# Kernel tuning notes

Hardware: AMD Instinct MI355X
Metric: run time of the kernel (lower is better)

## Reference

```python
import jax, jax.numpy as jnp
import numpy as np

N = 100000
E = 3200000
F_IN = 27
H1, C1 = 8, 8
H2, C2 = 1, 2
NEG_SLOPE = 0.2


def gat_conv(x, src, dst, W, a_src, a_dst, b, heads, ch, n_nodes):
    # x: [N, F_in]; src/dst: [E'] (self-loops already appended)
    h = (x @ W).reshape(n_nodes, heads, ch)            # [N, H, C]
    alpha_src = jnp.sum(h * a_src, axis=-1)            # [N, H]
    alpha_dst = jnp.sum(h * a_dst, axis=-1)            # [N, H]
    e = jax.nn.leaky_relu(alpha_src[src] + alpha_dst[dst], NEG_SLOPE)  # [E', H]
    m = jax.ops.segment_max(e, dst, num_segments=n_nodes)             # [N, H]
    ex = jnp.exp(e - m[dst])
    denom = jax.ops.segment_sum(ex, dst, num_segments=n_nodes)        # [N, H]
    alpha = ex / denom[dst]                                           # [E', H]
    out = jax.ops.segment_sum(h[src] * alpha[:, :, None], dst, num_segments=n_nodes)
    return out.reshape(n_nodes, heads * ch) + b


def setup_inputs() -> dict:
    key = jax.random.key(0)
    ks = jax.random.split(key, 10)
    x = jax.random.normal(ks[0], (N, F_IN), dtype=jnp.float32)
    edge_index = jax.random.randint(ks[1], (2, E), 0, N, dtype=jnp.int64)
    s1 = 1.0 / np.sqrt(F_IN)
    s2 = 1.0 / np.sqrt(H1 * C1)
    W1 = jax.random.uniform(ks[2], (F_IN, H1 * C1), jnp.float32, -s1, s1)
    a_src1 = jax.random.uniform(ks[3], (H1, C1), jnp.float32, -s1, s1)
    a_dst1 = jax.random.uniform(ks[4], (H1, C1), jnp.float32, -s1, s1)
    b1 = jnp.zeros((H1 * C1,), jnp.float32)
    W2 = jax.random.uniform(ks[5], (H1 * C1, H2 * C2), jnp.float32, -s2, s2)
    a_src2 = jax.random.uniform(ks[6], (H2, C2), jnp.float32, -s2, s2)
    a_dst2 = jax.random.uniform(ks[7], (H2, C2), jnp.float32, -s2, s2)
    b2 = jnp.zeros((H2 * C2,), jnp.float32)
    return {"x": x, "edge_index": edge_index, "W1": W1, "a_src1": a_src1,
            "a_dst1": a_dst1, "b1": b1, "W2": W2, "a_src2": a_src2,
            "a_dst2": a_dst2, "b2": b2}


def reference(x, edge_index, W1, a_src1, a_dst1, b1, W2, a_src2, a_dst2, b2):
    # eval mode: dropouts are identity. PyG GATConv adds self-loops by default.
    loop = jnp.arange(N, dtype=edge_index.dtype)
    src = jnp.concatenate([edge_index[0], loop])
    dst = jnp.concatenate([edge_index[1], loop])
    h = jax.nn.elu(gat_conv(x, src, dst, W1, a_src1, a_dst1, b1, H1, C1, N))
    out = gat_conv(h, src, dst, W2, a_src2, a_dst2, b2, H2, C2, N)
    return jax.nn.log_softmax(out, axis=1)
```

## Files before the change

### kernel.cpp

```cpp
#include <hip/hip_runtime.h>
#include <hip/hip_fp16.h>
#include <math.h>

#define NN 100000
#define EE 3200000
#define ET (EE + NN)

#define H1n 8
#define C1n 8
#define F1n 64
#define FINn 27
#define NEG 0.2f

#define NPB 128
#define NB 782
#define STRIDE 5120
#define TILE 4096
#define ABLK 256
#define WIN (STRIDE + NPB)
#define FBLK 512
#define RPT 10

typedef float floatx2 __attribute__((ext_vector_type(2)));

static __device__ __forceinline__ float lrelu(float v) {
    return v > 0.f ? v : NEG * v;
}

__global__ __launch_bounds__(ABLK) void k_binA(const int* __restrict__ ei,
                                               int* __restrict__ tail,
                                               int* __restrict__ recs) {
    __shared__ int hist[NB];
    __shared__ int lofs[NB];
    __shared__ int cur[NB];
    __shared__ int gpos[NB];
    __shared__ int sorted[TILE];
    __shared__ unsigned short sbkt[TILE];
    __shared__ int part[ABLK];

    int tid = threadIdx.x;
    long long e0 = (long long)blockIdx.x * TILE;
    int cnt = (int)min((long long)TILE, (long long)EE - e0);

    for (int i = tid; i < NB; i += ABLK) hist[i] = 0;
    __syncthreads();

    int ss[TILE / ABLK], dd[TILE / ABLK];
    #pragma unroll
    for (int k = 0; k < TILE / ABLK; ++k) {
        int idx = k * ABLK + tid;
        if (idx < cnt) {
            ss[k] = ei[e0 + idx];
            dd[k] = ei[EE + e0 + idx];
            atomicAdd(&hist[dd[k] >> 7], 1);
        }
    }
    __syncthreads();
    {
        const int CH = (NB + ABLK - 1) / ABLK;
        int beg = tid * CH, end = min(beg + CH, NB);
        int s = 0;
        for (int i = beg; i < end; ++i) s += hist[i];
        part[tid] = s;
        __syncthreads();
        for (int off = 1; off < ABLK; off <<= 1) {
            int add = (tid >= off) ? part[tid - off] : 0;
            __syncthreads();
            part[tid] += add;
            __syncthreads();
        }
        int ex = (tid > 0) ? part[tid - 1] : 0;
        for (int i = beg; i < end; ++i) {
            lofs[i] = ex;
            cur[i] = ex;
            ex += hist[i];
        }
    }
    __syncthreads();
    #pragma unroll
    for (int k = 0; k < TILE / ABLK; ++k) {
        int idx = k * ABLK + tid;
        if (idx < cnt) {
            int b = dd[k] >> 7;
            int r = atomicAdd(&cur[b], 1);
            sorted[r] = ss[k] | ((dd[k] & (NPB - 1)) << 17);
            sbkt[r] = (unsigned short)b;
        }
    }
    __syncthreads();
    for (int i = tid; i < NB; i += ABLK) {
        int c = hist[i];
        if (c > 0) gpos[i] = atomicAdd(&tail[i], c);
    }
    __syncthreads();
    for (int t = tid; t < cnt; t += ABLK) {
        int b = sbkt[t];
        recs[(size_t)b * STRIDE + gpos[b] + (t - lofs[b])] = sorted[t];
    }
}

__global__ __launch_bounds__(256) void k_h1(const float* __restrict__ x,
                                            const float* __restrict__ W1,
                                            const float* __restrict__ a_src1,
                                            const float* __restrict__ a_dst1,
                                            unsigned char* __restrict__ h1q,
                                            __half* __restrict__ as1h,
                                            float* __restrict__ ad1) {
    int gt = blockIdx.x * blockDim.x + threadIdx.x;
    int n = gt >> 6;
    if (n >= NN) return;
    int lane = threadIdx.x & 63;
    const float* xr = x + (size_t)n * FINn;
    float s = 0.f;
    #pragma unroll
    for (int k = 0; k < FINn; ++k) s = fmaf(xr[k], W1[k * F1n + lane], s);
    float s2 = __shfl_down(s, 1, 64);
    if (!(lane & 1)) {
        int pk = __builtin_amdgcn_cvt_pk_fp8_f32(s, s2, 0, false);
        ((unsigned short*)(h1q + (size_t)n * F1n))[lane >> 1] =
            (unsigned short)(pk & 0xFFFF);
    }
    float ps = s * a_src1[lane];
    float pd = s * a_dst1[lane];
    #pragma unroll
    for (int off = 1; off < 8; off <<= 1) {
        ps += __shfl_xor(ps, off, 64);
        pd += __shfl_xor(pd, off, 64);
    }
    if ((lane & 7) == 0) {
        int h = lane >> 3;
        as1h[n * H1n + h] = __float2half(ps);
        ad1[n * H1n + h] = pd;
    }
}

__global__ __launch_bounds__(FBLK) void k_f1(const int* __restrict__ recs,
                                             const int* __restrict__ tail,
                                             const unsigned* __restrict__ h1q,
                                             const __half* __restrict__ as1h,
                                             const float* __restrict__ ad1,
                                             const float* __restrict__ b1,
                                             const float* __restrict__ W2,
                                             const float* __restrict__ a_src2,
                                             const float* __restrict__ a_dst2,
                                             uint2* __restrict__ rec2,
                                             int* __restrict__ gwin,
                                             uint2* __restrict__ nrange) {
    __shared__ int hist[NPB];
    __shared__ int cur[NPB];
    __shared__ int rloc[NPB + 1];
    __shared__ int window[WIN];
    __shared__ int wtot[2];

    int b = blockIdx.x;
    int tid = threadIdx.x;
    int node0 = b * NPB;
    int nodes = min(NPB, NN - node0);
    int rcnt = tail[b];
    const int* rb = recs + (size_t)b * STRIDE;

    if (tid < NPB) hist[tid] = 0;
    __syncthreads();
    int rg[RPT];
    int nmine = 0;
    #pragma unroll
    for (int k = 0; k < RPT; ++k) {
        int i = tid + k * FBLK;
        if (i < rcnt) {
            rg[k] = rb[i];
            atomicAdd(&hist[rg[k] >> 17], 1);
            nmine = k + 1;
        }
    }
    __syncthreads();
    int v = 0, inc = 0;
    if (tid < NPB) {
        v = (tid < nodes) ? hist[tid] + 1 : 0;
        inc = v;
        #pragma unroll
        for (int off = 1; off < 64; off <<= 1) {
            int t = __shfl_up(inc, off, 64);
            if ((tid & 63) >= off) inc += t;
        }
        if ((tid & 63) == 63) wtot[tid >> 6] = inc;
    }
    __syncthreads();
    if (tid < NPB) {
        if (tid >= 64) inc += wtot[0];
        int ex = inc - v;
        if (tid < nodes) {
            rloc[tid] = ex;
            cur[tid] = ex + 1;
            window[ex] = node0 + tid;
        }
    }
    if (tid == 0) rloc[nodes] = wtot[0] + wtot[1];
    __syncthreads();
    #pragma unroll
    for (int k = 0; k < RPT; ++k) {
        if (k < nmine) {
            int r = rg[k];
            int p = atomicAdd(&cur[r >> 17], 1);
            window[p] = r & 0x1FFFF;
        }
    }
    __syncthreads();
    {
        int T = rloc[nodes];
        int gbase = b * WIN;
        for (int i = tid; i < T; i += FBLK)
            gwin[gbase + i] = window[i];
        if (tid < nodes) {
            uint2 r;
            r.x = (unsigned)(gbase + rloc[tid]);
            r.y = (unsigned)(gbase + rloc[tid + 1]);
            nrange[node0 + tid] = r;
        }
    }

    int lane = tid & 63;
    int wv = tid >> 6;
    int e8 = lane >> 3;
    int hh = lane & 7;
    int q = lane >> 4;
    int c4 = lane & 15;
    int bpe = e8 << 2;
    int bpq = q << 2;
    int bpx = ((q << 3) + (c4 >> 1)) << 2;

    for (int ln = wv; ln < nodes; ln += FBLK / 64) {
        int n = node0 + ln;
        float adh = ad1[(n << 3) + hh];
        int beg = rloc[ln], end = rloc[ln + 1];
        float a0 = 0.f, a1 = 0.f, a2 = 0.f, a3 = 0.f, den = 0.f;

        for (int base = beg; base < end; base += 64) {
            int cnt = min(64, end - base);
            int sidx = (lane < cnt) ? window[base + lane] : 0;
            for (int sb = 0; sb < cnt; sb += 8) {
                int sb4 = sb << 2;
                int s_sc = __builtin_amdgcn_ds_bpermute(sb4 + bpe, sidx);
                float A = __half2float(as1h[((unsigned)s_sc << 3) + hh]);
                float sc = A + adh;
                sc = fmaxf(sc, 0.2f * sc);
                float x = (sb + e8 < cnt) ? __expf(sc) : 0.f;
                den += x;
                int xi = __float_as_int(x);
                #pragma unroll
                for (int jj = 0; jj < 2; ++jj) {
                    int s_a = __builtin_amdgcn_ds_bpermute(sb4 + (jj << 4) + bpq, sidx);
                    int xr_ = __builtin_amdgcn_ds_bpermute((jj << 7) + bpx, xi);
                    float xv = __int_as_float(xr_);
                    unsigned dw = h1q[((unsigned)s_a << 4) + c4];
                    floatx2 lo = __builtin_amdgcn_cvt_pk_f32_fp8((int)dw, false);
                    floatx2 hi = __builtin_amdgcn_cvt_pk_f32_fp8((int)dw, true);
                    a0 = fmaf(xv, lo.x, a0);
                    a1 = fmaf(xv, lo.y, a1);
                    a2 = fmaf(xv, hi.x, a2);
                    a3 = fmaf(xv, hi.y, a3);
                }
            }
        }

        den += __shfl_xor(den, 8, 64);
        den += __shfl_xor(den, 16, 64);
        den += __shfl_xor(den, 32, 64);
        den = __int_as_float(
            __builtin_amdgcn_ds_bpermute((c4 >> 1) << 2, __float_as_int(den)));
        #pragma unroll
        for (int off = 16; off < 64; off <<= 1) {
            a0 += __shfl_xor(a0, off, 64);
            a1 += __shfl_xor(a1, off, 64);
            a2 += __shfl_xor(a2, off, 64);
            a3 += __shfl_xor(a3, off, 64);
        }
        float inv = 1.f / den;
        float v0 = a0 * inv + b1[c4 * 4 + 0];
        float v1 = a1 * inv + b1[c4 * 4 + 1];
        float v2 = a2 * inv + b1[c4 * 4 + 2];
        float v3 = a3 * inv + b1[c4 * 4 + 3];
        v0 = v0 > 0.f ? v0 : expm1f(v0);
        v1 = v1 > 0.f ? v1 : expm1f(v1);
        v2 = v2 > 0.f ? v2 : expm1f(v2);
        v3 = v3 > 0.f ? v3 : expm1f(v3);
        float p0 = v0 * W2[(c4 * 4 + 0) * 2 + 0] + v1 * W2[(c4 * 4 + 1) * 2 + 0] +
                   v2 * W2[(c4 * 4 + 2) * 2 + 0] + v3 * W2[(c4 * 4 + 3) * 2 + 0];
        float p1 = v0 * W2[(c4 * 4 + 0) * 2 + 1] + v1 * W2[(c4 * 4 + 1) * 2 + 1] +
                   v2 * W2[(c4 * 4 + 2) * 2 + 1] + v3 * W2[(c4 * 4 + 3) * 2 + 1];
        #pragma unroll
        for (int off = 1; off < 16; off <<= 1) {
            p0 += __shfl_xor(p0, off, 64);
            p1 += __shfl_xor(p1, off, 64);
        }
        if (lane == 0) {
            float as2 = p0 * a_src2[0] + p1 * a_src2[1];
            float ad2 = p0 * a_dst2[0] + p1 * a_dst2[1];
            __half2 lo2 = __floats2half2_rn(p0, p1);
            __half2 hi2 = __floats2half2_rn(as2, ad2);
            uint2 r;
            r.x = *(unsigned*)&lo2;
            r.y = *(unsigned*)&hi2;
            rec2[n] = r;
        }
    }
}

__global__ __launch_bounds__(256) void k_f2(const int* __restrict__ gwin,
                                            const uint2* __restrict__ nrange,
                                            const uint2* __restrict__ rec2,
                                            const float* __restrict__ b2,
                                            float* __restrict__ out) {
    int n = blockIdx.x * blockDim.x + threadIdx.x;
    if (n >= NN) return;
    __half2 mysd = *(const __half2*)&rec2[n].y;
    float adv = __half2float(__high2half(mysd));
    uint2 rr = nrange[n];
    float den = 0.f, a0 = 0.f, a1 = 0.f;
    for (unsigned i = rr.x; i < rr.y; ++i) {
        int s = gwin[i];
        uint2 rv = rec2[s];
        __half2 h01 = *(const __half2*)&rv.x;
        __half2 hsd = *(const __half2*)&rv.y;
        float e = lrelu(__half2float(__low2half(hsd)) + adv);
        float ex = __expf(e);
        den += ex;
        a0 = fmaf(ex, __half2float(__low2half(h01)), a0);
        a1 = fmaf(ex, __half2float(__high2half(h01)), a1);
    }
    float v0 = a0 / den + b2[0];
    float v1 = a1 / den + b2[1];
    float mx = fmaxf(v0, v1);
    float ls = mx + logf(__expf(v0 - mx) + __expf(v1 - mx));
    float2 o;
    o.x = v0 - ls;
    o.y = v1 - ls;
    ((float2*)out)[n] = o;
}

extern "C" void kernel_launch(void* const* d_in, const int* in_sizes, int n_in,
                              void* d_out, int out_size, void* d_ws, size_t ws_size,
                              hipStream_t stream) {
    const float* x      = (const float*)d_in[0];
    const int*   ei     = (const int*)d_in[1];
    const float* W1     = (const float*)d_in[2];
    const float* a_src1 = (const float*)d_in[3];
    const float* a_dst1 = (const float*)d_in[4];
    const float* b1     = (const float*)d_in[5];
    const float* W2     = (const float*)d_in[6];
    const float* a_src2 = (const float*)d_in[7];
    const float* a_dst2 = (const float*)d_in[8];
    const float* b2     = (const float*)d_in[9];
    float* out = (float*)d_out;

    char* wsb = (char*)d_ws;
    size_t o = 0;
    uint2* rec2 = (uint2*)wsb;                   o += (size_t)NN * 8;
    uint2* nrange = (uint2*)(wsb + o);           o += (size_t)NN * 8;
    #define ALLOC(name, type, count) type* name = (type*)(wsb + o); o += (size_t)(count) * 4;
    ALLOC(ad1,    float, NN * H1n)
    ALLOC(recs,   int,   (size_t)NB * STRIDE)
    ALLOC(gwin,   int,   (size_t)NB * WIN)
    ALLOC(tail,   int,   NB)
    #undef ALLOC
    __half* as1h = (__half*)(wsb + o);               o += (size_t)NN * H1n * 2;
    unsigned char* h1q = (unsigned char*)(wsb + o);  o += (size_t)NN * F1n;

    const int B = 256;
    #define GRID(n) ((unsigned)(((long long)(n) + B - 1) / B))

    hipMemsetAsync(tail, 0, (size_t)NB * sizeof(int), stream);
    k_binA<<<(EE + TILE - 1) / TILE, ABLK, 0, stream>>>(ei, tail, recs);

    k_h1<<<GRID((size_t)NN * 64), B, 0, stream>>>(x, W1, a_src1, a_dst1, h1q, as1h, ad1);

    k_f1<<<NB, FBLK, 0, stream>>>(recs, tail, (const unsigned*)h1q, as1h, ad1, b1,
                                  W2, a_src2, a_dst2, rec2, gwin, nrange);

    k_f2<<<GRID(NN), B, 0, stream>>>(gwin, nrange, rec2, b2, out);
    #undef GRID
}
```

Baseline: 217.1 us.

## Split layer-1 aggregation into two head-half passes and reuse atomic ranks in binning

The fp8 node features and half-precision source scores are split into two half-width arrays (heads 0-3 and heads 4-7). The aggregation kernel now makes two passes over each block's edges, one per half. This halves the gathered working set per pass so it fits better in L2/cache, at the cost of re-reading the edge window and doing the softmax bookkeeping twice. Per-node partial layer-2 projections from the first pass are kept in shared memory. Separately, the binning kernel reuses the rank returned by the histogram atomicAdd instead of doing a second atomic scatter pass, which removes one set of shared-memory atomics.

```diff
diff --git a/kernel.cpp b/kernel.cpp
--- a/kernel.cpp
+++ b/kernel.cpp
@@ -32,7 +32,6 @@
                                                int* __restrict__ recs) {
     __shared__ int hist[NB];
     __shared__ int lofs[NB];
-    __shared__ int cur[NB];
     __shared__ int gpos[NB];
     __shared__ int sorted[TILE];
     __shared__ unsigned short sbkt[TILE];
@@ -45,14 +44,14 @@
     for (int i = tid; i < NB; i += ABLK) hist[i] = 0;
     __syncthreads();
 
-    int ss[TILE / ABLK], dd[TILE / ABLK];
+    int ss[TILE / ABLK], dd[TILE / ABLK], rk[TILE / ABLK];
     #pragma unroll
     for (int k = 0; k < TILE / ABLK; ++k) {
         int idx = k * ABLK + tid;
         if (idx < cnt) {
             ss[k] = ei[e0 + idx];
             dd[k] = ei[EE + e0 + idx];
-            atomicAdd(&hist[dd[k] >> 7], 1);
+            rk[k] = atomicAdd(&hist[dd[k] >> 7], 1);
         }
     }
     __syncthreads();
@@ -72,7 +71,6 @@
         int ex = (tid > 0) ? part[tid - 1] : 0;
         for (int i = beg; i < end; ++i) {
             lofs[i] = ex;
-            cur[i] = ex;
             ex += hist[i];
         }
     }
@@ -82,7 +80,7 @@
         int idx = k * ABLK + tid;
         if (idx < cnt) {
             int b = dd[k] >> 7;
-            int r = atomicAdd(&cur[b], 1);
+            int r = lofs[b] + rk[k];
             sorted[r] = ss[k] | ((dd[k] & (NPB - 1)) << 17);
             sbkt[r] = (unsigned short)b;
         }
@@ -103,8 +101,10 @@
                                             const float* __restrict__ W1,
                                             const float* __restrict__ a_src1,
                                             const float* __restrict__ a_dst1,
-                                            unsigned char* __restrict__ h1q,
-                                            __half* __restrict__ as1h,
+                                            unsigned char* __restrict__ h1qA,
+                                            unsigned char* __restrict__ h1qB,
+                                            __half* __restrict__ as1hA,
+                                            __half* __restrict__ as1hB,
                                             float* __restrict__ ad1) {
     int gt = blockIdx.x * blockDim.x + threadIdx.x;
     int n = gt >> 6;
@@ -117,7 +117,8 @@
     float s2 = __shfl_down(s, 1, 64);
     if (!(lane & 1)) {
         int pk = __builtin_amdgcn_cvt_pk_fp8_f32(s, s2, 0, false);
-        ((unsigned short*)(h1q + (size_t)n * F1n))[lane >> 1] =
+        unsigned char* tb = (lane < 32) ? h1qA : h1qB;
+        ((unsigned short*)(tb + (size_t)n * 32))[(lane & 31) >> 1] =
             (unsigned short)(pk & 0xFFFF);
     }
     float ps = s * a_src1[lane];
@@ -129,15 +130,18 @@
     }
     if ((lane & 7) == 0) {
         int h = lane >> 3;
-        as1h[n * H1n + h] = __float2half(ps);
+        __half* ta = (h < 4) ? as1hA : as1hB;
+        ta[n * 4 + (h & 3)] = __float2half(ps);
         ad1[n * H1n + h] = pd;
     }
 }
 
 __global__ __launch_bounds__(FBLK) void k_f1(const int* __restrict__ recs,
                                              const int* __restrict__ tail,
-                                             const unsigned* __restrict__ h1q,
-                                             const __half* __restrict__ as1h,
+                                             const unsigned* __restrict__ h1qA,
+                                             const unsigned* __restrict__ h1qB,
+                                             const __half* __restrict__ as1hA,
+                                             const __half* __restrict__ as1hB,
                                              const float* __restrict__ ad1,
                                              const float* __restrict__ b1,
                                              const float* __restrict__ W2,
@@ -151,6 +155,7 @@
     __shared__ int rloc[NPB + 1];
     __shared__ int window[WIN];
     __shared__ int wtot[2];
+    __shared__ float2 part2[NPB];
 
     int b = blockIdx.x;
     int tid = threadIdx.x;
@@ -220,87 +225,104 @@
 
     int lane = tid & 63;
     int wv = tid >> 6;
-    int e8 = lane >> 3;
-    int hh = lane & 7;
-    int q = lane >> 4;
-    int c4 = lane & 15;
-    int bpe = e8 << 2;
-    int bpq = q << 2;
-    int bpx = ((q << 3) + (c4 >> 1)) << 2;
-
-    for (int ln = wv; ln < nodes; ln += FBLK / 64) {
-        int n = node0 + ln;
-        float adh = ad1[(n << 3) + hh];
-        int beg = rloc[ln], end = rloc[ln + 1];
-        float a0 = 0.f, a1 = 0.f, a2 = 0.f, a3 = 0.f, den = 0.f;
-
-        for (int base = beg; base < end; base += 64) {
-            int cnt = min(64, end - base);
-            int sidx = (lane < cnt) ? window[base + lane] : 0;
-            for (int sb = 0; sb < cnt; sb += 8) {
-                int sb4 = sb << 2;
-                int s_sc = __builtin_amdgcn_ds_bpermute(sb4 + bpe, sidx);
-                float A = __half2float(as1h[((unsigned)s_sc << 3) + hh]);
-                float sc = A + adh;
-                sc = fmaxf(sc, 0.2f * sc);
-                float x = (sb + e8 < cnt) ? __expf(sc) : 0.f;
-                den += x;
-                int xi = __float_as_int(x);
-                #pragma unroll
-                for (int jj = 0; jj < 2; ++jj) {
-                    int s_a = __builtin_amdgcn_ds_bpermute(sb4 + (jj << 4) + bpq, sidx);
-                    int xr_ = __builtin_amdgcn_ds_bpermute((jj << 7) + bpx, xi);
-                    float xv = __int_as_float(xr_);
-                    unsigned dw = h1q[((unsigned)s_a << 4) + c4];
-                    floatx2 lo = __builtin_amdgcn_cvt_pk_f32_fp8((int)dw, false);
-                    floatx2 hi = __builtin_amdgcn_cvt_pk_f32_fp8((int)dw, true);
-                    a0 = fmaf(xv, lo.x, a0);
-                    a1 = fmaf(xv, lo.y, a1);
-                    a2 = fmaf(xv, hi.x, a2);
-                    a3 = fmaf(xv, hi.y, a3);
+    int hh4 = lane & 3;
+    int c4h = lane & 7;
+    int bps = lane & 60;
+    int bpq = (lane >> 3) << 2;
+    int bpx = ((lane >> 3) << 4) + ((c4h >> 1) << 2);
+
+    #pragma unroll
+    for (int pass = 0; pass < 2; ++pass) {
+        const unsigned* h1h = pass ? h1qB : h1qA;
+        const __half* as1h = pass ? as1hB : as1hA;
+        int ch0 = pass * 32 + c4h * 4;
+        float bch0 = b1[ch0 + 0], bch1 = b1[ch0 + 1];
+        float bch2 = b1[ch0 + 2], bch3 = b1[ch0 + 3];
+        float w2a0 = W2[(ch0 + 0) * 2], w2b0 = W2[(ch0 + 0) * 2 + 1];
+        float w2a1 = W2[(ch0 + 1) * 2], w2b1 = W2[(ch0 + 1) * 2 + 1];
+        float w2a2 = W2[(ch0 + 2) * 2], w2b2 = W2[(ch0 + 2) * 2 + 1];
+        float w2a3 = W2[(ch0 + 3) * 2], w2b3 = W2[(ch0 + 3) * 2 + 1];
+
+        for (int ln = wv; ln < nodes; ln += FBLK / 64) {
+            int n = node0 + ln;
+            float adh = ad1[(n << 3) + (pass << 2) + hh4];
+            int beg = rloc[ln], end = rloc[ln + 1];
+            float a0 = 0.f, a1 = 0.f, a2 = 0.f, a3 = 0.f, den = 0.f;
+
+            for (int base = beg; base < end; base += 64) {
+                int cnt = min(64, end - base);
+                int sidx = (lane < cnt) ? window[base + lane] : 0;
+                for (int sb = 0; sb < cnt; sb += 16) {
+                    int sb4 = sb << 2;
+                    int s_sc = __builtin_amdgcn_ds_bpermute(sb4 + bps, sidx);
+                    float A = __half2float(as1h[((unsigned)s_sc << 2) + hh4]);
+                    float sc = A + adh;
+                    sc = fmaxf(sc, 0.2f * sc);
+                    float x = (sb + (lane >> 2) < cnt) ? __expf(sc) : 0.f;
+                    den += x;
+                    int xi = __float_as_int(x);
+                    #pragma unroll
+                    for (int jj = 0; jj < 2; ++jj) {
+                        int s_a = __builtin_amdgcn_ds_bpermute(
+                            sb4 + (jj << 5) + bpq, sidx);
+                        int xr_ = __builtin_amdgcn_ds_bpermute((jj << 7) + bpx, xi);
+                        float xv = __int_as_float(xr_);
+                        unsigned dw = h1h[((unsigned)s_a << 3) + c4h];
+                        floatx2 lo = __builtin_amdgcn_cvt_pk_f32_fp8((int)dw, false);
+                        floatx2 hi = __builtin_amdgcn_cvt_pk_f32_fp8((int)dw, true);
+                        a0 = fmaf(xv, lo.x, a0);
+                        a1 = fmaf(xv, lo.y, a1);
+                        a2 = fmaf(xv, hi.x, a2);
+                        a3 = fmaf(xv, hi.y, a3);
+                    }
                 }
             }
-        }
-
-        den += __shfl_xor(den, 8, 64);
-        den += __shfl_xor(den, 16, 64);
-        den += __shfl_xor(den, 32, 64);
-        den = __int_as_float(
-            __builtin_amdgcn_ds_bpermute((c4 >> 1) << 2, __float_as_int(den)));
-        #pragma unroll
-        for (int off = 16; off < 64; off <<= 1) {
-            a0 += __shfl_xor(a0, off, 64);
-            a1 += __shfl_xor(a1, off, 64);
-            a2 += __shfl_xor(a2, off, 64);
-            a3 += __shfl_xor(a3, off, 64);
-        }
-        float inv = 1.f / den;
-        float v0 = a0 * inv + b1[c4 * 4 + 0];
-        float v1 = a1 * inv + b1[c4 * 4 + 1];
-        float v2 = a2 * inv + b1[c4 * 4 + 2];
-        float v3 = a3 * inv + b1[c4 * 4 + 3];
-        v0 = v0 > 0.f ? v0 : expm1f(v0);
-        v1 = v1 > 0.f ? v1 : expm1f(v1);
-        v2 = v2 > 0.f ? v2 : expm1f(v2);
-        v3 = v3 > 0.f ? v3 : expm1f(v3);
-        float p0 = v0 * W2[(c4 * 4 + 0) * 2 + 0] + v1 * W2[(c4 * 4 + 1) * 2 + 0] +
-                   v2 * W2[(c4 * 4 + 2) * 2 + 0] + v3 * W2[(c4 * 4 + 3) * 2 + 0];
-        float p1 = v0 * W2[(c4 * 4 + 0) * 2 + 1] + v1 * W2[(c4 * 4 + 1) * 2 + 1] +
-                   v2 * W2[(c4 * 4 + 2) * 2 + 1] + v3 * W2[(c4 * 4 + 3) * 2 + 1];
-        #pragma unroll
-        for (int off = 1; off < 16; off <<= 1) {
-            p0 += __shfl_xor(p0, off, 64);
-            p1 += __shfl_xor(p1, off, 64);
-        }
-        if (lane == 0) {
-            float as2 = p0 * a_src2[0] + p1 * a_src2[1];
-            float ad2 = p0 * a_dst2[0] + p1 * a_dst2[1];
-            __half2 lo2 = __floats2half2_rn(p0, p1);
-            __half2 hi2 = __floats2half2_rn(as2, ad2);
-            uint2 r;
-            r.x = *(unsigned*)&lo2;
-            r.y = *(unsigned*)&hi2;
-            rec2[n] = r;
+
+            den += __shfl_xor(den, 4, 64);
+            den += __shfl_xor(den, 8, 64);
+            den += __shfl_xor(den, 16, 64);
+            den += __shfl_xor(den, 32, 64);
+            den = __int_as_float(__builtin_amdgcn_ds_bpermute(
+                (c4h >> 1) << 2, __float_as_int(den)));
+            #pragma unroll
+            for (int off = 8; off < 64; off <<= 1) {
+                a0 += __shfl_xor(a0, off, 64);
+                a1 += __shfl_xor(a1, off, 64);
+                a2 += __shfl_xor(a2, off, 64);
+                a3 += __shfl_xor(a3, off, 64);
+            }
+            float inv = 1.f / den;
+            float v0 = a0 * inv + bch0;
+            float v1 = a1 * inv + bch1;
+            float v2 = a2 * inv + bch2;
+            float v3 = a3 * inv + bch3;
+            v0 = v0 > 0.f ? v0 : expm1f(v0);
+            v1 = v1 > 0.f ? v1 : expm1f(v1);
+            v2 = v2 > 0.f ? v2 : expm1f(v2);
+            v3 = v3 > 0.f ? v3 : expm1f(v3);
+            float p0 = v0 * w2a0 + v1 * w2a1 + v2 * w2a2 + v3 * w2a3;
+            float p1 = v0 * w2b0 + v1 * w2b1 + v2 * w2b2 + v3 * w2b3;
+            p0 += __shfl_xor(p0, 1, 64);
+            p1 += __shfl_xor(p1, 1, 64);
+            p0 += __shfl_xor(p0, 2, 64);
+            p1 += __shfl_xor(p1, 2, 64);
+            p0 += __shfl_xor(p0, 4, 64);
+            p1 += __shfl_xor(p1, 4, 64);
+            if (pass == 0) {
+                if (lane == 0) part2[ln] = make_float2(p0, p1);
+            } else if (lane == 0) {
+                float2 pp = part2[ln];
+                p0 += pp.x;
+                p1 += pp.y;
+                float as2 = p0 * a_src2[0] + p1 * a_src2[1];
+                float ad2 = p0 * a_dst2[0] + p1 * a_dst2[1];
+                __half2 lo2 = __floats2half2_rn(p0, p1);
+                __half2 hi2 = __floats2half2_rn(as2, ad2);
+                uint2 r;
+                r.x = *(unsigned*)&lo2;
+                r.y = *(unsigned*)&hi2;
+                rec2[n] = r;
+            }
         }
     }
 }
@@ -362,8 +384,10 @@
     ALLOC(gwin,   int,   (size_t)NB * WIN)
     ALLOC(tail,   int,   NB)
     #undef ALLOC
-    __half* as1h = (__half*)(wsb + o);               o += (size_t)NN * H1n * 2;
-    unsigned char* h1q = (unsigned char*)(wsb + o);  o += (size_t)NN * F1n;
+    __half* as1hA = (__half*)(wsb + o);              o += (size_t)NN * 4 * 2;
+    __half* as1hB = (__half*)(wsb + o);              o += (size_t)NN * 4 * 2;
+    unsigned char* h1qA = (unsigned char*)(wsb + o); o += (size_t)NN * 32;
+    unsigned char* h1qB = (unsigned char*)(wsb + o); o += (size_t)NN * 32;
 
     const int B = 256;
     #define GRID(n) ((unsigned)(((long long)(n) + B - 1) / B))
@@ -371,9 +395,11 @@
     hipMemsetAsync(tail, 0, (size_t)NB * sizeof(int), stream);
     k_binA<<<(EE + TILE - 1) / TILE, ABLK, 0, stream>>>(ei, tail, recs);
 
-    k_h1<<<GRID((size_t)NN * 64), B, 0, stream>>>(x, W1, a_src1, a_dst1, h1q, as1h, ad1);
-
-    k_f1<<<NB, FBLK, 0, stream>>>(recs, tail, (const unsigned*)h1q, as1h, ad1, b1,
+    k_h1<<<GRID((size_t)NN * 64), B, 0, stream>>>(x, W1, a_src1, a_dst1,
+                                                  h1qA, h1qB, as1hA, as1hB, ad1);
+
+    k_f1<<<NB, FBLK, 0, stream>>>(recs, tail, (const unsigned*)h1qA,
+                                  (const unsigned*)h1qB, as1hA, as1hB, ad1, b1,
                                   W2, a_src2, a_dst2, rec2, gwin, nrange);
 
     k_f2<<<GRID(NN), B, 0, stream>>>(gwin, nrange, rec2, b2, out);
```

Measured after the change: 258.1 us. +18.9%, slower.

## Split fused sort+aggregate kernel into sort and per-node message-passing kernels

Applied to the files above, without the earlier changes.

Splits the k_f1 kernel into k_sort, which builds the per-bucket CSR windows in LDS and writes them out, and k_mp, where one wavefront handles one destination node and reads neighbor indices from global gwin. The fused version held 128 nodes per 512-thread block with about 21KB of LDS, which limited occupancy and caused tail imbalance. The split version is meant to give finer-grained, better-balanced work in the aggregation phase. In exchange it adds an extra launch and a global re-read of the window. Separately, k_binA now reuses the rank returned by the histogram atomic instead of doing a second atomic pass on a cur array.

```diff
diff --git a/kernel.cpp b/kernel.cpp
--- a/kernel.cpp
+++ b/kernel.cpp
@@ -32,7 +32,6 @@
                                                int* __restrict__ recs) {
     __shared__ int hist[NB];
     __shared__ int lofs[NB];
-    __shared__ int cur[NB];
     __shared__ int gpos[NB];
     __shared__ int sorted[TILE];
     __shared__ unsigned short sbkt[TILE];
@@ -45,14 +44,14 @@
     for (int i = tid; i < NB; i += ABLK) hist[i] = 0;
     __syncthreads();
 
-    int ss[TILE / ABLK], dd[TILE / ABLK];
+    int ss[TILE / ABLK], dd[TILE / ABLK], rk[TILE / ABLK];
     #pragma unroll
     for (int k = 0; k < TILE / ABLK; ++k) {
         int idx = k * ABLK + tid;
         if (idx < cnt) {
             ss[k] = ei[e0 + idx];
             dd[k] = ei[EE + e0 + idx];
-            atomicAdd(&hist[dd[k] >> 7], 1);
+            rk[k] = atomicAdd(&hist[dd[k] >> 7], 1);
         }
     }
     __syncthreads();
@@ -72,7 +71,6 @@
         int ex = (tid > 0) ? part[tid - 1] : 0;
         for (int i = beg; i < end; ++i) {
             lofs[i] = ex;
-            cur[i] = ex;
             ex += hist[i];
         }
     }
@@ -82,7 +80,7 @@
         int idx = k * ABLK + tid;
         if (idx < cnt) {
             int b = dd[k] >> 7;
-            int r = atomicAdd(&cur[b], 1);
+            int r = lofs[b] + rk[k];
             sorted[r] = ss[k] | ((dd[k] & (NPB - 1)) << 17);
             sbkt[r] = (unsigned short)b;
         }
@@ -134,18 +132,10 @@
     }
 }
 
-__global__ __launch_bounds__(FBLK) void k_f1(const int* __restrict__ recs,
-                                             const int* __restrict__ tail,
-                                             const unsigned* __restrict__ h1q,
-                                             const __half* __restrict__ as1h,
-                                             const float* __restrict__ ad1,
-                                             const float* __restrict__ b1,
-                                             const float* __restrict__ W2,
-                                             const float* __restrict__ a_src2,
-                                             const float* __restrict__ a_dst2,
-                                             uint2* __restrict__ rec2,
-                                             int* __restrict__ gwin,
-                                             uint2* __restrict__ nrange) {
+__global__ __launch_bounds__(FBLK) void k_sort(const int* __restrict__ recs,
+                                               const int* __restrict__ tail,
+                                               int* __restrict__ gwin,
+                                               uint2* __restrict__ nrange) {
     __shared__ int hist[NPB];
     __shared__ int cur[NPB];
     __shared__ int rloc[NPB + 1];
@@ -205,21 +195,31 @@
         }
     }
     __syncthreads();
-    {
-        int T = rloc[nodes];
-        int gbase = b * WIN;
-        for (int i = tid; i < T; i += FBLK)
-            gwin[gbase + i] = window[i];
-        if (tid < nodes) {
-            uint2 r;
-            r.x = (unsigned)(gbase + rloc[tid]);
-            r.y = (unsigned)(gbase + rloc[tid + 1]);
-            nrange[node0 + tid] = r;
-        }
-    }
-
-    int lane = tid & 63;
-    int wv = tid >> 6;
+    int T = rloc[nodes];
+    int gbase = b * WIN;
+    for (int i = tid; i < T; i += FBLK)
+        gwin[gbase + i] = window[i];
+    if (tid < nodes) {
+        uint2 r;
+        r.x = (unsigned)(gbase + rloc[tid]);
+        r.y = (unsigned)(gbase + rloc[tid + 1]);
+        nrange[node0 + tid] = r;
+    }
+}
+
+__global__ __launch_bounds__(FBLK) void k_mp(const int* __restrict__ gwin,
+                                             const uint2* __restrict__ nrange,
+                                             const unsigned* __restrict__ h1q,
+                                             const __half* __restrict__ as1h,
+                                             const float* __restrict__ ad1,
+                                             const float* __restrict__ b1,
+                                             const float* __restrict__ W2,
+                                             const float* __restrict__ a_src2,
+                                             const float* __restrict__ a_dst2,
+                                             uint2* __restrict__ rec2) {
+    int n = (int)(((unsigned)blockIdx.x * FBLK + threadIdx.x) >> 6);
+    if (n >= NN) return;
+    int lane = threadIdx.x & 63;
     int e8 = lane >> 3;
     int hh = lane & 7;
     int q = lane >> 4;
@@ -228,80 +228,77 @@
     int bpq = q << 2;
     int bpx = ((q << 3) + (c4 >> 1)) << 2;
 
-    for (int ln = wv; ln < nodes; ln += FBLK / 64) {
-        int n = node0 + ln;
-        float adh = ad1[(n << 3) + hh];
-        int beg = rloc[ln], end = rloc[ln + 1];
-        float a0 = 0.f, a1 = 0.f, a2 = 0.f, a3 = 0.f, den = 0.f;
-
-        for (int base = beg; base < end; base += 64) {
-            int cnt = min(64, end - base);
-            int sidx = (lane < cnt) ? window[base + lane] : 0;
-            for (int sb = 0; sb < cnt; sb += 8) {
-                int sb4 = sb << 2;
-                int s_sc = __builtin_amdgcn_ds_bpermute(sb4 + bpe, sidx);
-                float A = __half2float(as1h[((unsigned)s_sc << 3) + hh]);
-                float sc = A + adh;
-                sc = fmaxf(sc, 0.2f * sc);
-                float x = (sb + e8 < cnt) ? __expf(sc) : 0.f;
-                den += x;
-                int xi = __float_as_int(x);
-                #pragma unroll
-                for (int jj = 0; jj < 2; ++jj) {
-                    int s_a = __builtin_amdgcn_ds_bpermute(sb4 + (jj << 4) + bpq, sidx);
-                    int xr_ = __builtin_amdgcn_ds_bpermute((jj << 7) + bpx, xi);
-                    float xv = __int_as_float(xr_);
-                    unsigned dw = h1q[((unsigned)s_a << 4) + c4];
-                    floatx2 lo = __builtin_amdgcn_cvt_pk_f32_fp8((int)dw, false);
-                    floatx2 hi = __builtin_amdgcn_cvt_pk_f32_fp8((int)dw, true);
-                    a0 = fmaf(xv, lo.x, a0);
-                    a1 = fmaf(xv, lo.y, a1);
-                    a2 = fmaf(xv, hi.x, a2);
-                    a3 = fmaf(xv, hi.y, a3);
-                }
+    float adh = ad1[(n << 3) + hh];
+    uint2 rr = nrange[n];
+    float a0 = 0.f, a1 = 0.f, a2 = 0.f, a3 = 0.f, den = 0.f;
+
+    for (unsigned base = rr.x; base < rr.y; base += 64) {
+        int cnt = (int)min(64u, rr.y - base);
+        int sidx = (lane < cnt) ? gwin[base + lane] : 0;
+        for (int sb = 0; sb < cnt; sb += 8) {
+            int sb4 = sb << 2;
+            int s_sc = __builtin_amdgcn_ds_bpermute(sb4 + bpe, sidx);
+            float A = __half2float(as1h[((unsigned)s_sc << 3) + hh]);
+            float sc = A + adh;
+            sc = fmaxf(sc, 0.2f * sc);
+            float x = (sb + e8 < cnt) ? __expf(sc) : 0.f;
+            den += x;
+            int xi = __float_as_int(x);
+            #pragma unroll
+            for (int jj = 0; jj < 2; ++jj) {
+                int s_a = __builtin_amdgcn_ds_bpermute(sb4 + (jj << 4) + bpq, sidx);
+                int xr_ = __builtin_amdgcn_ds_bpermute((jj << 7) + bpx, xi);
+                float xv = __int_as_float(xr_);
+                unsigned dw = h1q[((unsigned)s_a << 4) + c4];
+                floatx2 lo = __builtin_amdgcn_cvt_pk_f32_fp8((int)dw, false);
+                floatx2 hi = __builtin_amdgcn_cvt_pk_f32_fp8((int)dw, true);
+                a0 = fmaf(xv, lo.x, a0);
+                a1 = fmaf(xv, lo.y, a1);
+                a2 = fmaf(xv, hi.x, a2);
+                a3 = fmaf(xv, hi.y, a3);
             }
         }
-
-        den += __shfl_xor(den, 8, 64);
-        den += __shfl_xor(den, 16, 64);
-        den += __shfl_xor(den, 32, 64);
-        den = __int_as_float(
-            __builtin_amdgcn_ds_bpermute((c4 >> 1) << 2, __float_as_int(den)));
-        #pragma unroll
-        for (int off = 16; off < 64; off <<= 1) {
-            a0 += __shfl_xor(a0, off, 64);
-            a1 += __shfl_xor(a1, off, 64);
-            a2 += __shfl_xor(a2, off, 64);
-            a3 += __shfl_xor(a3, off, 64);
-        }
-        float inv = 1.f / den;
-        float v0 = a0 * inv + b1[c4 * 4 + 0];
-        float v1 = a1 * inv + b1[c4 * 4 + 1];
-        float v2 = a2 * inv + b1[c4 * 4 + 2];
-        float v3 = a3 * inv + b1[c4 * 4 + 3];
-        v0 = v0 > 0.f ? v0 : expm1f(v0);
-        v1 = v1 > 0.f ? v1 : expm1f(v1);
-        v2 = v2 > 0.f ? v2 : expm1f(v2);
-        v3 = v3 > 0.f ? v3 : expm1f(v3);
-        float p0 = v0 * W2[(c4 * 4 + 0) * 2 + 0] + v1 * W2[(c4 * 4 + 1) * 2 + 0] +
-                   v2 * W2[(c4 * 4 + 2) * 2 + 0] + v3 * W2[(c4 * 4 + 3) * 2 + 0];
-        float p1 = v0 * W2[(c4 * 4 + 0) * 2 + 1] + v1 * W2[(c4 * 4 + 1) * 2 + 1] +
-                   v2 * W2[(c4 * 4 + 2) * 2 + 1] + v3 * W2[(c4 * 4 + 3) * 2 + 1];
-        #pragma unroll
-        for (int off = 1; off < 16; off <<= 1) {
-            p0 += __shfl_xor(p0, off, 64);
-            p1 += __shfl_xor(p1, off, 64);
-        }
-        if (lane == 0) {
-            float as2 = p0 * a_src2[0] + p1 * a_src2[1];
-            float ad2 = p0 * a_dst2[0] + p1 * a_dst2[1];
-            __half2 lo2 = __floats2half2_rn(p0, p1);
-            __half2 hi2 = __floats2half2_rn(as2, ad2);
-            uint2 r;
-            r.x = *(unsigned*)&lo2;
-            r.y = *(unsigned*)&hi2;
-            rec2[n] = r;
-        }
+    }
+
+    den += __shfl_xor(den, 8, 64);
+    den += __shfl_xor(den, 16, 64);
+    den += __shfl_xor(den, 32, 64);
+    den = __int_as_float(
+        __builtin_amdgcn_ds_bpermute((c4 >> 1) << 2, __float_as_int(den)));
+    #pragma unroll
+    for (int off = 16; off < 64; off <<= 1) {
+        a0 += __shfl_xor(a0, off, 64);
+        a1 += __shfl_xor(a1, off, 64);
+        a2 += __shfl_xor(a2, off, 64);
+        a3 += __shfl_xor(a3, off, 64);
+    }
+    float inv = 1.f / den;
+    float v0 = a0 * inv + b1[c4 * 4 + 0];
+    float v1 = a1 * inv + b1[c4 * 4 + 1];
+    float v2 = a2 * inv + b1[c4 * 4 + 2];
+    float v3 = a3 * inv + b1[c4 * 4 + 3];
+    v0 = v0 > 0.f ? v0 : expm1f(v0);
+    v1 = v1 > 0.f ? v1 : expm1f(v1);
+    v2 = v2 > 0.f ? v2 : expm1f(v2);
+    v3 = v3 > 0.f ? v3 : expm1f(v3);
+    float p0 = v0 * W2[(c4 * 4 + 0) * 2 + 0] + v1 * W2[(c4 * 4 + 1) * 2 + 0] +
+               v2 * W2[(c4 * 4 + 2) * 2 + 0] + v3 * W2[(c4 * 4 + 3) * 2 + 0];
+    float p1 = v0 * W2[(c4 * 4 + 0) * 2 + 1] + v1 * W2[(c4 * 4 + 1) * 2 + 1] +
+               v2 * W2[(c4 * 4 + 2) * 2 + 1] + v3 * W2[(c4 * 4 + 3) * 2 + 1];
+    #pragma unroll
+    for (int off = 1; off < 16; off <<= 1) {
+        p0 += __shfl_xor(p0, off, 64);
+        p1 += __shfl_xor(p1, off, 64);
+    }
+    if (lane == 0) {
+        float as2 = p0 * a_src2[0] + p1 * a_src2[1];
+        float ad2 = p0 * a_dst2[0] + p1 * a_dst2[1];
+        __half2 lo2 = __floats2half2_rn(p0, p1);
+        __half2 hi2 = __floats2half2_rn(as2, ad2);
+        uint2 r;
+        r.x = *(unsigned*)&lo2;
+        r.y = *(unsigned*)&hi2;
+        rec2[n] = r;
     }
 }
 
@@ -373,8 +370,10 @@
 
     k_h1<<<GRID((size_t)NN * 64), B, 0, stream>>>(x, W1, a_src1, a_dst1, h1q, as1h, ad1);
 
-    k_f1<<<NB, FBLK, 0, stream>>>(recs, tail, (const unsigned*)h1q, as1h, ad1, b1,
-                                  W2, a_src2, a_dst2, rec2, gwin, nrange);
+    k_sort<<<NB, FBLK, 0, stream>>>(recs, tail, gwin, nrange);
+
+    k_mp<<<(unsigned)(((size_t)NN * 64 + FBLK - 1) / FBLK), FBLK, 0, stream>>>(
+        gwin, nrange, (const unsigned*)h1q, as1h, ad1, b1, W2, a_src2, a_dst2, rec2);
 
     k_f2<<<GRID(NN), B, 0, stream>>>(gwin, nrange, rec2, b2, out);
     #undef GRID
```

Result: faster. 211.3 us (-2.6%).
